# Performance work log

Measured on AMD Instinct MI355X. Metric: run time of the kernel, lower is better.

## Reference

```python
import jax, jax.numpy as jnp
import numpy as np

RADIUS = 5
KS = 2 * RADIUS + 1  # 11
SIGMA_X2 = 4.0 ** 2  # 16
SIGMA_I2 = 10.0 ** 2  # 100


def _patches(x):
    """x: [N,1,H,W] -> [N, H*W, KS, KS] zero-padded sliding windows (torch Unfold semantics)."""
    N, _, H, W = x.shape
    p = jax.lax.conv_general_dilated_patches(
        x, (KS, KS), (1, 1), [(RADIUS, RADIUS), (RADIUS, RADIUS)]
    )  # [N, KS*KS, H, W], channel dim ordered (kh, kw)
    return p.reshape(N, KS, KS, H * W).transpose(0, 3, 1, 2)


def _distance_map(dtype):
    d = (jnp.arange(KS, dtype=dtype) - RADIUS) ** 2
    return jnp.exp(-(d[:, None] + d[None, :]) / SIGMA_X2)  # [KS, KS]


def setup_inputs() -> dict:
    key = jax.random.key(0)
    k1, k2 = jax.random.split(key)
    images = jax.random.uniform(k1, (8, 1, 224, 224), dtype=jnp.float32)
    labels = jax.random.uniform(k2, (8, 4, 224, 224), dtype=jnp.float32)
    return {"images": images, "labels": labels}


def reference(images, labels):
    B, _, H, W = images.shape
    K = labels.shape[1]
    HW = H * W

    img = images * 255.0
    regions = _patches(img)                                   # [B,HW,KS,KS]
    mask = _patches(jnp.ones((1, 1, H, W), img.dtype))        # [1,HW,KS,KS], 0 on padding
    dist_map = _distance_map(img.dtype)                       # [KS,KS]

    i_f = img.reshape(B, HW)[:, :, None, None]                # center pixel intensity
    weights = dist_map * jnp.exp(-(regions - i_f) ** 2 / SIGMA_I2) * mask  # [B,HW,KS,KS]

    # class-prob patches for all classes at once
    P = _patches(labels.reshape(B * K, 1, H, W)).reshape(B, K, HW, KS, KS)

    num = jnp.einsum('bnij,bknij->bkn', weights, P)           # sum_j w_ij * p_j
    den = weights.sum(axis=(2, 3))                            # [B,HW], sum_j w_ij
    p_f = labels.reshape(B, K, HW)

    ratio = jnp.einsum('bkn,bkn->bk', p_f, num) / jnp.einsum('bkn,bn->bk', p_f, den)
    # per-class L1Loss(ratio, 0) = mean over batch of |ratio|; summed over classes
    ratio_sum = jnp.abs(ratio).mean(axis=0).sum()
    return K - ratio_sum
```

## Files before the change

kernel.cpp:

```cpp
#include <hip/hip_runtime.h>
#include <type_traits>

typedef float f2 __attribute__((ext_vector_type(2)));
typedef float f4 __attribute__((ext_vector_type(4)));

constexpr int Hh = 224, Ww = 224, Bb = 8, Kc = 4, RAD = 5;

constexpr int TX = 32;
constexpr int TILEH = 16;
constexpr int NTHR = 512;
constexpr int SW = TX + 2 * RAD;
constexpr int SH = TILEH + 2 * RAD;
constexpr int SSTR = SW + 1;
constexpr int GXD = Ww / TX;
constexpr int GYD = Hh / TILEH;
constexpr int PB = GXD * GYD;

constexpr float LOG2E = 1.44269504f;
constexpr float KI = -0.01f * LOG2E;
constexpr float DSC = -0.0625f * LOG2E;
constexpr float D2[12] = {25.f,16.f,9.f,4.f,1.f,0.f,1.f,4.f,9.f,16.f,25.f,1e5f};

static __device__ inline f4 splat4(float x) { return (f4){x, x, x, x}; }

__global__ __launch_bounds__(NTHR, 6) void ncut_main(const float* __restrict__ images,
                                                     const float* __restrict__ labels,
                                                     float* __restrict__ acc) {
    __shared__ float simg[SH * SSTR];
    __shared__ f4    slab[SH * SSTR];
    __shared__ float red[8][8];

    const int b   = blockIdx.z;
    const int x0  = blockIdx.x * TX;
    const int y0  = blockIdx.y * TILEH;
    const int tid = threadIdx.x;

    const float* imgb = images + (size_t)b * (Hh * Ww);
    const float* labb = labels + (size_t)b * (Kc * Hh * Ww);

    for (int idx = tid; idx < SH * SSTR; idx += NTHR) {
        const int lx = idx % SSTR, ly = idx / SSTR;
        const int gx = x0 - RAD + lx, gy = y0 - RAD + ly;
        float iv = 1e19f;
        f4 lv = (f4){0.f, 0.f, 0.f, 0.f};
        if (lx < SW && gx >= 0 && gx < Ww && gy >= 0 && gy < Hh) {
            const int g = gy * Ww + gx;
            iv = imgb[g] * 255.0f;
            lv = (f4){labb[g], labb[Hh * Ww + g], labb[2 * Hh * Ww + g], labb[3 * Hh * Ww + g]};
        }
        simg[idx] = iv;
        slab[idx] = lv;
    }
    __syncthreads();

    const int tx  = tid & 31;
    const int ty  = (tid >> 5) & 7;
    const int grp = tid >> 8;
    const int r0  = 2 * ty;

    const float c0 = simg[(r0 + RAD) * SSTR + tx + RAD];
    const float c1 = simg[(r0 + RAD + 1) * SSTR + tx + RAD];

    f4 num0 = splat4(0.f), num1 = splat4(0.f);
    f2 den0 = (f2){0.f, 0.f}, den1 = (f2){0.f, 0.f};

    auto body = [&](auto GC) {
        constexpr int G = decltype(GC)::value;
#pragma unroll
        for (int d = 0; d < 6; ++d) {
            const int dr = 6 * G + d;
            const int rowoff = (r0 + dr) * SSTR + tx;
#pragma unroll
            for (int i = 0; i < 6; ++i) {
                const f2 v  = (f2){simg[rowoff + 2 * i], simg[rowoff + 2 * i + 1]};
                const f4 p0 = slab[rowoff + 2 * i];
                const f4 p1 = slab[rowoff + 2 * i + 1];
                if (dr < 11) {
                    const f2 base = (f2){(D2[2 * i] + D2[dr]) * DSC,
                                         (D2[2 * i + 1] + D2[dr]) * DSC};
                    const f2 dd = v - c0;
                    const f2 a = __builtin_elementwise_fma(dd * KI, dd, base);
                    const float e0 = __builtin_amdgcn_exp2f(a.x);
                    const float e1 = __builtin_amdgcn_exp2f(a.y);
                    den0 += (f2){e0, e1};
                    num0 = __builtin_elementwise_fma(splat4(e0), p0, num0);
                    num0 = __builtin_elementwise_fma(splat4(e1), p1, num0);
                }
                if (dr >= 1) {
                    const f2 base = (f2){(D2[2 * i] + D2[dr - 1]) * DSC,
                                         (D2[2 * i + 1] + D2[dr - 1]) * DSC};
                    const f2 dd = v - c1;
                    const f2 a = __builtin_elementwise_fma(dd * KI, dd, base);
                    const float e0 = __builtin_amdgcn_exp2f(a.x);
                    const float e1 = __builtin_amdgcn_exp2f(a.y);
                    den1 += (f2){e0, e1};
                    num1 = __builtin_elementwise_fma(splat4(e0), p0, num1);
                    num1 = __builtin_elementwise_fma(splat4(e1), p1, num1);
                }
            }
        }
    };
    if (grp == 0) body(std::integral_constant<int, 0>{});
    else          body(std::integral_constant<int, 1>{});

    const f4 pc0 = slab[(r0 + RAD) * SSTR + tx + RAD];
    const f4 pc1 = slab[(r0 + RAD + 1) * SSTR + tx + RAD];
    const float dn0 = den0.x + den0.y;
    const float dn1 = den1.x + den1.y;

    const f4 numv = pc0 * num0 + pc1 * num1;
    const f4 denv = pc0 * dn0 + pc1 * dn1;

    float vals[8] = {numv.x, numv.y, numv.z, numv.w, denv.x, denv.y, denv.z, denv.w};

#pragma unroll
    for (int i = 0; i < 8; ++i) {
        float v = vals[i];
#pragma unroll
        for (int off = 32; off > 0; off >>= 1) v += __shfl_down(v, off, 64);
        vals[i] = v;
    }

    const int wave = tid >> 6, lane = tid & 63;
    if (lane == 0) {
#pragma unroll
        for (int i = 0; i < 8; ++i) red[wave][i] = vals[i];
    }
    __syncthreads();

    if (tid < 8) {
        const int gid = blockIdx.x + GXD * blockIdx.y + GXD * GYD * blockIdx.z;
        float s = 0.f;
#pragma unroll
        for (int w = 0; w < 8; ++w) s += red[w][tid];
        acc[gid * 8 + tid] = s;
    }
}

__global__ void ncut_final(const float* __restrict__ acc, float* __restrict__ out) {
    __shared__ float red[4][64];
    const int t = threadIdx.x;
    const int combo = t & 63;
    const int chunk = t >> 6;
    const int k = combo & 3, b = (combo >> 2) & 7;
    const int part = combo >> 5;
    float s = 0.f;
    for (int j = chunk; j < PB; j += 4)
        s += acc[(b * PB + j) * 8 + k + 4 * part];
    red[chunk][combo] = s;
    __syncthreads();
    if (t < 64) {
        float v = red[0][t] + red[1][t] + red[2][t] + red[3][t];
        const float den = __shfl(v, (t + 32) & 63, 64);
        float r = (t < 32) ? fabsf(v / den) : 0.f;
#pragma unroll
        for (int off = 32; off > 0; off >>= 1) r += __shfl_down(r, off, 64);
        if (t == 0) out[0] = (float)Kc - r * (1.0f / (float)Bb);
    }
}

extern "C" void kernel_launch(void* const* d_in, const int* in_sizes, int n_in,
                              void* d_out, int out_size, void* d_ws, size_t ws_size,
                              hipStream_t stream) {
    const float* images = (const float*)d_in[0];
    const float* labels = (const float*)d_in[1];
    float* out = (float*)d_out;
    float* acc = (float*)d_ws;

    dim3 grid(GXD, GYD, Bb);
    ncut_main<<<grid, NTHR, 0, stream>>>(images, labels, acc);
    ncut_final<<<1, 256, 0, stream>>>(acc, out);
}
```

Before: 89.50 us.

## Process four output rows per thread and pack labels as fp16 in shared memory

Each thread now computes four vertically adjacent output pixels instead of two, with the tile height doubled. A single loaded window row is therefore reused across more center pixels, which cuts LDS traffic per output. Image values and fp16-packed label pairs are stored together in one f4 shared-memory record, so one wide load returns both. The exchange is higher register pressure, reflected in the occupancy hint dropping from 6 to 4, plus fp16 rounding of label probabilities that could slightly change the result.

Result: faster. 85.67 us (-4.3%).

```diff
diff --git a/kernel.cpp b/kernel.cpp
--- a/kernel.cpp
+++ b/kernel.cpp
@@ -3,11 +3,12 @@
 
 typedef float f2 __attribute__((ext_vector_type(2)));
 typedef float f4 __attribute__((ext_vector_type(4)));
+typedef _Float16 h2t __attribute__((ext_vector_type(2)));
 
 constexpr int Hh = 224, Ww = 224, Bb = 8, Kc = 4, RAD = 5;
 
 constexpr int TX = 32;
-constexpr int TILEH = 16;
+constexpr int TILEH = 32;
 constexpr int NTHR = 512;
 constexpr int SW = TX + 2 * RAD;
 constexpr int SH = TILEH + 2 * RAD;
@@ -23,11 +24,19 @@
 
 static __device__ inline f4 splat4(float x) { return (f4){x, x, x, x}; }
 
-__global__ __launch_bounds__(NTHR, 6) void ncut_main(const float* __restrict__ images,
+static __device__ inline float pack2(float a, float b) {
+    return __builtin_bit_cast(float, __builtin_amdgcn_cvt_pkrtz(a, b));
+}
+static __device__ inline f4 unpack4(float y, float z) {
+    const h2t a = __builtin_bit_cast(h2t, y);
+    const h2t b = __builtin_bit_cast(h2t, z);
+    return (f4){(float)a.x, (float)a.y, (float)b.x, (float)b.y};
+}
+
+__global__ __launch_bounds__(NTHR, 4) void ncut_main(const float* __restrict__ images,
                                                      const float* __restrict__ labels,
                                                      float* __restrict__ acc) {
-    __shared__ float simg[SH * SSTR];
-    __shared__ f4    slab[SH * SSTR];
+    __shared__ f4 stap[SH * SSTR];
     __shared__ float red[8][8];
 
     const int b   = blockIdx.z;
@@ -41,61 +50,61 @@
     for (int idx = tid; idx < SH * SSTR; idx += NTHR) {
         const int lx = idx % SSTR, ly = idx / SSTR;
         const int gx = x0 - RAD + lx, gy = y0 - RAD + ly;
-        float iv = 1e19f;
-        f4 lv = (f4){0.f, 0.f, 0.f, 0.f};
+        float iv = 1e19f, p01 = 0.f, p23 = 0.f;
         if (lx < SW && gx >= 0 && gx < Ww && gy >= 0 && gy < Hh) {
             const int g = gy * Ww + gx;
-            iv = imgb[g] * 255.0f;
-            lv = (f4){labb[g], labb[Hh * Ww + g], labb[2 * Hh * Ww + g], labb[3 * Hh * Ww + g]};
+            iv  = imgb[g] * 255.0f;
+            p01 = pack2(labb[g], labb[Hh * Ww + g]);
+            p23 = pack2(labb[2 * Hh * Ww + g], labb[3 * Hh * Ww + g]);
         }
-        simg[idx] = iv;
-        slab[idx] = lv;
+        stap[idx] = (f4){iv, p01, p23, 0.f};
     }
     __syncthreads();
 
     const int tx  = tid & 31;
     const int ty  = (tid >> 5) & 7;
     const int grp = tid >> 8;
-    const int r0  = 2 * ty;
+    const int r0  = 4 * ty;
 
-    const float c0 = simg[(r0 + RAD) * SSTR + tx + RAD];
-    const float c1 = simg[(r0 + RAD + 1) * SSTR + tx + RAD];
+    f4 crec[4];
+    float c[4];
+#pragma unroll
+    for (int p = 0; p < 4; ++p) {
+        crec[p] = stap[(r0 + p + RAD) * SSTR + tx + RAD];
+        c[p] = crec[p].x;
+    }
 
-    f4 num0 = splat4(0.f), num1 = splat4(0.f);
-    f2 den0 = (f2){0.f, 0.f}, den1 = (f2){0.f, 0.f};
+    f4 num[4];
+    f2 den[4];
+#pragma unroll
+    for (int p = 0; p < 4; ++p) { num[p] = splat4(0.f); den[p] = (f2){0.f, 0.f}; }
 
     auto body = [&](auto GC) {
         constexpr int G = decltype(GC)::value;
 #pragma unroll
-        for (int d = 0; d < 6; ++d) {
-            const int dr = 6 * G + d;
+        for (int d = 0; d < 7; ++d) {
+            const int dr = 7 * G + d;
             const int rowoff = (r0 + dr) * SSTR + tx;
 #pragma unroll
             for (int i = 0; i < 6; ++i) {
-                const f2 v  = (f2){simg[rowoff + 2 * i], simg[rowoff + 2 * i + 1]};
-                const f4 p0 = slab[rowoff + 2 * i];
-                const f4 p1 = slab[rowoff + 2 * i + 1];
-                if (dr < 11) {
-                    const f2 base = (f2){(D2[2 * i] + D2[dr]) * DSC,
-                                         (D2[2 * i + 1] + D2[dr]) * DSC};
-                    const f2 dd = v - c0;
-                    const f2 a = __builtin_elementwise_fma(dd * KI, dd, base);
-                    const float e0 = __builtin_amdgcn_exp2f(a.x);
-                    const float e1 = __builtin_amdgcn_exp2f(a.y);
-                    den0 += (f2){e0, e1};
-                    num0 = __builtin_elementwise_fma(splat4(e0), p0, num0);
-                    num0 = __builtin_elementwise_fma(splat4(e1), p1, num0);
-                }
-                if (dr >= 1) {
-                    const f2 base = (f2){(D2[2 * i] + D2[dr - 1]) * DSC,
-                                         (D2[2 * i + 1] + D2[dr - 1]) * DSC};
-                    const f2 dd = v - c1;
-                    const f2 a = __builtin_elementwise_fma(dd * KI, dd, base);
-                    const float e0 = __builtin_amdgcn_exp2f(a.x);
-                    const float e1 = __builtin_amdgcn_exp2f(a.y);
-                    den1 += (f2){e0, e1};
-                    num1 = __builtin_elementwise_fma(splat4(e0), p0, num1);
-                    num1 = __builtin_elementwise_fma(splat4(e1), p1, num1);
+                const f4 rA = stap[rowoff + 2 * i];
+                const f4 rB = stap[rowoff + 2 * i + 1];
+                const f2 v  = (f2){rA.x, rB.x};
+                const f4 a0 = unpack4(rA.y, rA.z);
+                const f4 a1 = unpack4(rB.y, rB.z);
+#pragma unroll
+                for (int p = 0; p < 4; ++p) {
+                    if (dr >= p && dr <= p + 10) {
+                        const f2 base = (f2){(D2[2 * i] + D2[dr - p]) * DSC,
+                                             (D2[2 * i + 1] + D2[dr - p]) * DSC};
+                        const f2 dd = v - c[p];
+                        const f2 a = __builtin_elementwise_fma(dd * KI, dd, base);
+                        const float e0 = __builtin_amdgcn_exp2f(a.x);
+                        const float e1 = __builtin_amdgcn_exp2f(a.y);
+                        den[p] += (f2){e0, e1};
+                        num[p] = __builtin_elementwise_fma(splat4(e0), a0, num[p]);
+                        num[p] = __builtin_elementwise_fma(splat4(e1), a1, num[p]);
+                    }
                 }
             }
         }
@@ -103,13 +112,14 @@
     if (grp == 0) body(std::integral_constant<int, 0>{});
     else          body(std::integral_constant<int, 1>{});
 
-    const f4 pc0 = slab[(r0 + RAD) * SSTR + tx + RAD];
-    const f4 pc1 = slab[(r0 + RAD + 1) * SSTR + tx + RAD];
-    const float dn0 = den0.x + den0.y;
-    const float dn1 = den1.x + den1.y;
-
-    const f4 numv = pc0 * num0 + pc1 * num1;
-    const f4 denv = pc0 * dn0 + pc1 * dn1;
+    f4 numv = splat4(0.f), denv = splat4(0.f);
+#pragma unroll
+    for (int p = 0; p < 4; ++p) {
+        const f4 pc = unpack4(crec[p].y, crec[p].z);
+        const float dn = den[p].x + den[p].y;
+        numv = __builtin_elementwise_fma(pc, num[p], numv);
+        denv = __builtin_elementwise_fma(pc, splat4(dn), denv);
+    }
 
     float vals[8] = {numv.x, numv.y, numv.z, numv.w, denv.x, denv.y, denv.z, denv.w};
 
```
